# Kernel optimization log

Hardware: AMD Instinct MI355X
Metric: run time of the kernel (lower is better)

The kernel has to match this reference:

```python
import jax, jax.numpy as jnp
import numpy as np

N, D = 131072, 256


def setup_inputs() -> dict:
    key = jax.random.key(0)
    k1, k2 = jax.random.split(key)
    query_emb = jax.random.normal(k1, (N, D), dtype=jnp.float32)
    doc_emb = jax.random.normal(k2, (N, D), dtype=jnp.float32)
    return {"query_emb": query_emb, "doc_emb": doc_emb}


def reference(query_emb, doc_emb):
    # Original: -diag(Q @ D.T) reshaped to (N, 1).
    # diag(Q @ D.T)[i] == sum_k Q[i,k] * D[i,k], so compute the row-wise
    # dot product directly (O(N*d) instead of O(N^2*d)).
    sim_score = -jnp.sum(query_emb * doc_emb, axis=1, keepdims=True)  # [N, 1]
    return sim_score
```

## Files before the change

### kernel.cpp

```cpp
#include <hip/hip_runtime.h>


constexpr int kN = 131072;
constexpr int kD = 256;

__global__ __launch_bounds__(256) void neg_rowdot_kernel(
    const float* __restrict__ q, const float* __restrict__ d,
    float* __restrict__ out, int n_rows) {
  const int gwave = (blockIdx.x * blockDim.x + threadIdx.x) >> 6;
  const int lane = threadIdx.x & 63;
  const int nwaves = (gridDim.x * blockDim.x) >> 6;

  for (int row = gwave; row < n_rows; row += nwaves) {
    const float4* qr = reinterpret_cast<const float4*>(q + (size_t)row * kD);
    const float4* dr = reinterpret_cast<const float4*>(d + (size_t)row * kD);
    const float4 a = qr[lane];
    const float4 b = dr[lane];
    float s = a.x * b.x + a.y * b.y + a.z * b.z + a.w * b.w;
#pragma unroll
    for (int off = 32; off; off >>= 1) s += __shfl_xor(s, off, 64);
    if (lane == 0) out[row] = -s;
  }
}

extern "C" void kernel_launch(void* const* d_in, const int* in_sizes, int n_in,
                              void* d_out, int out_size, void* d_ws, size_t ws_size,
                              hipStream_t stream) {
  const float* q = reinterpret_cast<const float*>(d_in[0]);
  const float* d = reinterpret_cast<const float*>(d_in[1]);
  float* out = reinterpret_cast<float*>(d_out);

  neg_rowdot_kernel<<<2048, 256, 0, stream>>>(q, d, out, kN);
}
```

Before: 272.5 us.

## Process 16 rows per wave with batched loads and transposed shuffle reduction

```diff
diff --git a/kernel.cpp b/kernel.cpp
--- a/kernel.cpp
+++ b/kernel.cpp
@@ -2,33 +2,61 @@
 
 
 constexpr int kN = 131072;
-constexpr int kD = 256;
+constexpr int kD4 = 64;
+
+template <int MASK>
+__device__ __forceinline__ float merge2(float a, float b, int lane) {
+  float t = (lane & MASK) ? a : b;
+  float u = __shfl_xor(t, MASK, 64);
+  return ((lane & MASK) ? b : a) + u;
+}
 
 __global__ __launch_bounds__(256) void neg_rowdot_kernel(
-    const float* __restrict__ q, const float* __restrict__ d,
-    float* __restrict__ out, int n_rows) {
+    const float4* __restrict__ q, const float4* __restrict__ d,
+    float* __restrict__ out) {
   const int gwave = (blockIdx.x * blockDim.x + threadIdx.x) >> 6;
   const int lane = threadIdx.x & 63;
-  const int nwaves = (gridDim.x * blockDim.x) >> 6;
 
-  for (int row = gwave; row < n_rows; row += nwaves) {
-    const float4* qr = reinterpret_cast<const float4*>(q + (size_t)row * kD);
-    const float4* dr = reinterpret_cast<const float4*>(d + (size_t)row * kD);
-    const float4 a = qr[lane];
-    const float4 b = dr[lane];
-    float s = a.x * b.x + a.y * b.y + a.z * b.z + a.w * b.w;
+  const size_t base = (size_t)gwave * 16;
+
 #pragma unroll
-    for (int off = 32; off; off >>= 1) s += __shfl_xor(s, off, 64);
-    if (lane == 0) out[row] = -s;
+  for (int half = 0; half < 2; ++half) {
+    const size_t r0 = base + half * 8;
+
+    float4 qa[8], da[8];
+#pragma unroll
+    for (int r = 0; r < 8; ++r) {
+      qa[r] = q[(r0 + r) * kD4 + lane];
+      da[r] = d[(r0 + r) * kD4 + lane];
+    }
+
+    float s[8];
+#pragma unroll
+    for (int r = 0; r < 8; ++r)
+      s[r] = qa[r].x * da[r].x + qa[r].y * da[r].y + qa[r].z * da[r].z +
+             qa[r].w * da[r].w;
+
+    float m01 = merge2<1>(s[0], s[1], lane);
+    float m23 = merge2<1>(s[2], s[3], lane);
+    float m45 = merge2<1>(s[4], s[5], lane);
+    float m67 = merge2<1>(s[6], s[7], lane);
+    float m03 = merge2<2>(m01, m23, lane);
+    float m47 = merge2<2>(m45, m67, lane);
+    float m07 = merge2<4>(m03, m47, lane);
+    m07 += __shfl_xor(m07, 8, 64);
+    m07 += __shfl_xor(m07, 16, 64);
+    m07 += __shfl_xor(m07, 32, 64);
+
+    if (lane < 8) out[r0 + lane] = -m07;
   }
 }
 
 extern "C" void kernel_launch(void* const* d_in, const int* in_sizes, int n_in,
                               void* d_out, int out_size, void* d_ws, size_t ws_size,
                               hipStream_t stream) {
-  const float* q = reinterpret_cast<const float*>(d_in[0]);
-  const float* d = reinterpret_cast<const float*>(d_in[1]);
+  const float4* q = reinterpret_cast<const float4*>(d_in[0]);
+  const float4* d = reinterpret_cast<const float4*>(d_in[1]);
   float* out = reinterpret_cast<float*>(d_out);
 
-  neg_rowdot_kernel<<<2048, 256, 0, stream>>>(q, d, out, kN);
+  neg_rowdot_kernel<<<2048, 256, 0, stream>>>(q, d, out);
 }
```

New measurement: 275.0 us. About the same (+0.9%).

## Split rows across four lanes with deep hand-pipelined inline-asm loads

Applied to the files above, without the earlier changes.

```diff
diff --git a/kernel.cpp b/kernel.cpp
--- a/kernel.cpp
+++ b/kernel.cpp
@@ -1,26 +1,80 @@
 #include <hip/hip_runtime.h>
 
 
-constexpr int kN = 131072;
-constexpr int kD = 256;
+typedef float f4 __attribute__((ext_vector_type(4)));
+
+#define GLD(dst, ptr, OFFSTR)                                       \
+  asm volatile("global_load_dwordx4 %0, %1, off offset:" OFFSTR     \
+               : "=v"(dst)                                          \
+               : "v"(ptr))
+
+#define VWAIT(NSTR)                                                 \
+  do {                                                              \
+    asm volatile("s_waitcnt vmcnt(" NSTR ")" ::: "memory");         \
+    __builtin_amdgcn_sched_barrier(0);                              \
+  } while (0)
+
+#define DOT4ACC(acc, a, b)                                          \
+  acc += a.x * b.x + a.y * b.y + a.z * b.z + a.w * b.w
 
 __global__ __launch_bounds__(256) void neg_rowdot_kernel(
     const float* __restrict__ q, const float* __restrict__ d,
-    float* __restrict__ out, int n_rows) {
-  const int gwave = (blockIdx.x * blockDim.x + threadIdx.x) >> 6;
-  const int lane = threadIdx.x & 63;
-  const int nwaves = (gridDim.x * blockDim.x) >> 6;
+    float* __restrict__ out) {
+  const int tid = blockIdx.x * 256 + threadIdx.x;
+  const int row = tid >> 2;
+  const int chunk = tid & 3;
 
-  for (int row = gwave; row < n_rows; row += nwaves) {
-    const float4* qr = reinterpret_cast<const float4*>(q + (size_t)row * kD);
-    const float4* dr = reinterpret_cast<const float4*>(d + (size_t)row * kD);
-    const float4 a = qr[lane];
-    const float4 b = dr[lane];
-    float s = a.x * b.x + a.y * b.y + a.z * b.z + a.w * b.w;
-#pragma unroll
-    for (int off = 32; off; off >>= 1) s += __shfl_xor(s, off, 64);
-    if (lane == 0) out[row] = -s;
-  }
+  const float* qp = q + ((size_t)row * 256 + chunk * 64);
+  const float* dp = d + ((size_t)row * 256 + chunk * 64);
+
+  f4 qv[16], dv[16];
+
+  GLD(qv[0], qp, "0");    GLD(dv[0], dp, "0");
+  GLD(qv[1], qp, "16");   GLD(dv[1], dp, "16");
+  GLD(qv[2], qp, "32");   GLD(dv[2], dp, "32");
+  GLD(qv[3], qp, "48");   GLD(dv[3], dp, "48");
+  GLD(qv[4], qp, "64");   GLD(dv[4], dp, "64");
+  GLD(qv[5], qp, "80");   GLD(dv[5], dp, "80");
+  GLD(qv[6], qp, "96");   GLD(dv[6], dp, "96");
+  GLD(qv[7], qp, "112");  GLD(dv[7], dp, "112");
+
+  VWAIT("8");
+  float a0 = 0.f, a1 = 0.f, a2 = 0.f, a3 = 0.f;
+  GLD(qv[8], qp, "128");  GLD(dv[8], dp, "128");
+  GLD(qv[9], qp, "144");  GLD(dv[9], dp, "144");
+  GLD(qv[10], qp, "160"); GLD(dv[10], dp, "160");
+  GLD(qv[11], qp, "176"); GLD(dv[11], dp, "176");
+  DOT4ACC(a0, qv[0], dv[0]);
+  DOT4ACC(a1, qv[1], dv[1]);
+  DOT4ACC(a2, qv[2], dv[2]);
+  DOT4ACC(a3, qv[3], dv[3]);
+
+  VWAIT("8");
+  GLD(qv[12], qp, "192"); GLD(dv[12], dp, "192");
+  GLD(qv[13], qp, "208"); GLD(dv[13], dp, "208");
+  GLD(qv[14], qp, "224"); GLD(dv[14], dp, "224");
+  GLD(qv[15], qp, "240"); GLD(dv[15], dp, "240");
+  DOT4ACC(a0, qv[4], dv[4]);
+  DOT4ACC(a1, qv[5], dv[5]);
+  DOT4ACC(a2, qv[6], dv[6]);
+  DOT4ACC(a3, qv[7], dv[7]);
+
+  VWAIT("8");
+  DOT4ACC(a0, qv[8], dv[8]);
+  DOT4ACC(a1, qv[9], dv[9]);
+  DOT4ACC(a2, qv[10], dv[10]);
+  DOT4ACC(a3, qv[11], dv[11]);
+
+  VWAIT("0");
+  DOT4ACC(a0, qv[12], dv[12]);
+  DOT4ACC(a1, qv[13], dv[13]);
+  DOT4ACC(a2, qv[14], dv[14]);
+  DOT4ACC(a3, qv[15], dv[15]);
+
+  float s = (a0 + a1) + (a2 + a3);
+  s += __shfl_xor(s, 1, 64);
+  s += __shfl_xor(s, 2, 64);
+  if ((tid & 3) == 0) out[row] = -s;
 }
 
 extern "C" void kernel_launch(void* const* d_in, const int* in_sizes, int n_in,
@@ -30,5 +84,5 @@
   const float* d = reinterpret_cast<const float*>(d_in[1]);
   float* out = reinterpret_cast<float*>(d_out);
 
-  neg_rowdot_kernel<<<2048, 256, 0, stream>>>(q, d, out, kN);
+  neg_rowdot_kernel<<<2048, 256, 0, stream>>>(q, d, out);
 }
```

Result: slower. 280.9 us (+3.1%).
